# Kernel tuning notes

Hardware: AMD Instinct MI355X
Metric: run time of the kernel (lower is better)

## Reference

```python
import jax, jax.numpy as jnp
import numpy as np

B, S, H, C = 512, 16, 501, 7


def _uniform(k, shape, scale):
    return jax.random.uniform(k, shape, minval=-scale, maxval=scale, dtype=jnp.float32)


def setup_inputs() -> dict:
    key = jax.random.key(0)
    ks = jax.random.split(key, 20)
    s = 1.0 / np.sqrt(H)        # torch default init bound for Linear(H, .) and GRUCell
    se = 1.0 / np.sqrt(2 * H)   # Linear(2H, 1)
    z = jax.random.normal(ks[0], (B, H), jnp.float32)
    # strictly-lower-triangular 0/1 adjacency (DAG, ancestors have smaller index)
    dep = jax.random.randint(ks[1], (B, S, S), 0, 2).astype(jnp.float32)
    dep_graph = dep * jnp.tril(jnp.ones((S, S), jnp.float32), k=-1)
    node_encoding = jax.nn.one_hot(jax.random.randint(ks[2], (B, S), 0, C), C, dtype=jnp.float32)
    return {
        "z": z,
        "dep_graph": dep_graph,
        "node_encoding": node_encoding,
        "W_lin1": _uniform(ks[3], (H, H), s), "b_lin1": _uniform(ks[4], (H,), s),
        "W_vert": _uniform(ks[5], (C, H), s), "b_vert": _uniform(ks[6], (C,), s),
        "W_edge": _uniform(ks[7], (1, 2 * H), se), "b_edge": _uniform(ks[8], (1,), se),
        "W_gate": _uniform(ks[9], (H, H), s), "b_gate": _uniform(ks[10], (H,), s),
        "W_map": _uniform(ks[11], (H, H), s), "b_map": _uniform(ks[12], (H,), s),
        "W_ih": _uniform(ks[13], (3 * H, C), s), "b_ih": _uniform(ks[14], (3 * H,), s),
        "W_hh": _uniform(ks[15], (3 * H, H), s), "b_hh": _uniform(ks[16], (3 * H,), s),
    }


def _forward(z, dep_graph, node_encoding, W_lin1, b_lin1, W_vert, b_vert, W_edge, b_edge,
             W_gate, b_gate, W_map, b_map, W_ih, b_ih, W_hh, b_hh):
    Bs, Ss, _ = dep_graph.shape
    Hs = W_lin1.shape[0]

    def gru(x, h):  # torch.nn.GRUCell math
        gi = x @ W_ih.T + b_ih
        gh = h @ W_hh.T + b_hh
        i_r, i_z, i_n = jnp.split(gi, 3, axis=-1)
        h_r, h_z, h_n = jnp.split(gh, 3, axis=-1)
        r = jax.nn.sigmoid(i_r + h_r)
        u = jax.nn.sigmoid(i_z + h_z)
        n = jnp.tanh(i_n + r * h_n)
        return (1.0 - u) * n + u * h

    col = jnp.arange(Ss)

    def outer_step(carry, idx):
        graph_state, nhs = carry  # nhs: (B, S, H) node_hidden_state
        logits = jax.nn.softmax(graph_state @ W_vert.T + b_vert, axis=-1)  # add_vertex
        x_idx = jax.lax.dynamic_index_in_dim(node_encoding, idx, axis=1, keepdims=False)  # (B, C)
        row0 = jax.lax.dynamic_index_in_dim(dep_graph, idx, axis=1, keepdims=False)       # (B, S)

        def inner_step(ic, t):  # v_j = idx-1, ..., 0 (masked when v_j < 0)
            hv, nhs_i, row, edges = ic
            v_j = idx - 1 - t
            active = v_j >= 0
            vj = jnp.maximum(v_j, 0)
            hidden_j = jax.lax.dynamic_index_in_dim(nhs_i, vj, axis=1, keepdims=False)  # (B, H)
            p = jax.nn.sigmoid(jnp.concatenate([hv, hidden_j], axis=-1) @ W_edge.T + b_edge)  # (B,1)
            is_edge = (p[:, 0] >= 0.5).astype(z.dtype)  # hard threshold, as in source
            # emulates the in-place `ancestors[:, :v_j] = 0` on the dep_graph row
            row_new = jnp.where(col[None, :] < vj, 0.0, row)
            anc = (nhs_i * row_new[:, :, None]).reshape(-1, Hs)  # (B*S, H)
            h_in = (jax.nn.sigmoid(anc @ W_gate.T + b_gate) * (anc @ W_map.T + b_map)
                    ).reshape(Bs, Ss, Hs).sum(axis=1)  # gated-sum message aggregation
            hv_new = gru(x_idx, h_in)
            nhs_new = jax.lax.dynamic_update_index_in_dim(nhs_i, hv_new, idx, axis=1)
            edges = jnp.where(active, edges.at[:, vj].set(is_edge), edges)
            hv = jnp.where(active, hv_new, hv)
            nhs_i = jnp.where(active, nhs_new, nhs_i)
            row = jnp.where(active, row_new, row)
            return (hv, nhs_i, row, edges), None

        edges0 = jnp.zeros((Bs, Ss), z.dtype)
        (hv, nhs2, _, edges), _ = jax.lax.scan(
            inner_step, (graph_state, nhs, row0, edges0), jnp.arange(Ss - 1))
        # index == 0: no ancestors; hv = GRU(x_0, graph_state) (source leaves hv undefined here)
        hv = jnp.where(idx == 0, gru(x_idx, graph_state), hv)
        nhs3 = jax.lax.dynamic_update_index_in_dim(nhs2, hv, idx, axis=1)
        return (hv, nhs3), (logits, edges)

    graph_state0 = z @ W_lin1.T + b_lin1
    nhs0 = jnp.zeros((Bs, Ss, Hs), z.dtype)
    _, (enc, rows) = jax.lax.scan(outer_step, (graph_state0, nhs0), jnp.arange(Ss))
    gen_dep_graph = jnp.transpose(rows, (1, 0, 2))      # (B, S, S)
    gen_node_encoding = jnp.transpose(enc, (1, 0, 2))   # (B, S, C)
    return gen_dep_graph, gen_node_encoding


def reference(z, dep_graph, node_encoding, W_lin1, b_lin1, W_vert, b_vert, W_edge, b_edge,
              W_gate, b_gate, W_map, b_map, W_ih, b_ih, W_hh, b_hh):
    return _forward(z, dep_graph, node_encoding, W_lin1, b_lin1, W_vert, b_vert, W_edge,
                    b_edge, W_gate, b_gate, W_map, b_map, W_ih, b_ih, W_hh, b_hh)
```

## Files before the change

kernel.cpp:

```cpp
#include <hip/hip_runtime.h>
#include <math.h>

#define BB 512
#define SS 16
#define HH 501
#define CC 7
#define OFF_ENC (BB*SS*SS)

#define NBLK 256
#define NTHR 128
#define NTOT (NBLK*NTHR)
#define NBAR 34

#define O_ALIST 0
#define O_ELIST 8192
#define O_CLS   16384
#define O_SYNC  24576
#define O_WLIN  40960
#define O_WPOST (O_WLIN + 262144)
#define O_WHH   (O_WPOST + 524288)
#define O_WDOT  (O_WHH + 786432)
#define O_ROT   (O_WDOT + 8192)
#define SLOT_STRIDE 524288
#define SLOT_Z  0
#define SLOT_IN(t) (1 + (t))
#define SLOT_H(t)  (18 + (t))

typedef __attribute__((ext_vector_type(8))) short bfrag;
typedef __attribute__((ext_vector_type(4))) float ffrag;

__device__ __forceinline__ float sigm(float x) { return 1.f / (1.f + expf(-x)); }

__device__ __forceinline__ unsigned short f2bf(float x) {
    unsigned u = __float_as_uint(x);
    u = u + 0x7fffu + ((u >> 16) & 1u);
    return (unsigned short)(u >> 16);
}
__device__ __forceinline__ float bf2f(unsigned short h) {
    return __uint_as_float(((unsigned)h) << 16);
}

__device__ __forceinline__ void gridbar(int* __restrict__ bars, int id) {
    __syncthreads();
    int* f = bars + id * NBLK;
    if (threadIdx.x == 0)
        __hip_atomic_store(&f[blockIdx.x], 1, __ATOMIC_RELEASE, __HIP_MEMORY_SCOPE_AGENT);
    if (threadIdx.x < 64) {
        for (int i = threadIdx.x; i < NBLK; i += 64)
            while (__hip_atomic_load(&f[i], __ATOMIC_RELAXED, __HIP_MEMORY_SCOPE_AGENT) == 0)
                __builtin_amdgcn_s_sleep(2);
    }
    __syncthreads();
    asm volatile("" ::: "memory");
}

__global__ void k_init(int* bars, int n) {
    int i = blockIdx.x * 256 + threadIdx.x;
    if (i < n) bars[i] = 0;
}

__device__ __forceinline__ void wprep_item(
    int id,
    const float* __restrict__ Wlin1, const float* __restrict__ Wgate,
    const float* __restrict__ Wmap,  const float* __restrict__ Whh,
    const float* __restrict__ Wedge, const float* __restrict__ Wvert,
    unsigned short* __restrict__ wlin, unsigned short* __restrict__ wpost,
    unsigned short* __restrict__ whhf, unsigned short* __restrict__ wdot)
{
    const int slot = id >> 10, rem = id & 1023, s = rem >> 6, lane = rem & 63;
    const int rloc = lane & 15;
    const int k0 = s * 32 + ((lane >> 4) << 3);
    const float* src; unsigned short* dst; int dslot; bool valid;
    if (slot < 32) {
        int row = slot * 16 + rloc; valid = row < HH;
        src = Wlin1 + (size_t)(valid ? row : 0) * HH; dst = wlin; dslot = slot;
    } else if (slot < 96) {
        int p = slot - 32, g = p >> 5, mt = p & 31;
        int row = mt * 16 + rloc; valid = row < HH;
        src = (g ? Wmap : Wgate) + (size_t)(valid ? row : 0) * HH; dst = wpost; dslot = p;
    } else if (slot < 192) {
        int p = slot - 96, g = p >> 5, mt = p & 31;
        int row = mt * 16 + rloc; valid = row < HH;
        src = Whh + (size_t)(g * HH + (valid ? row : 0)) * HH; dst = whhf; dslot = p;
    } else {
        int row = rloc; dst = wdot; dslot = 0;
        if (row < 2)      { src = Wedge + (size_t)row * HH; valid = true; }
        else if (row < 9) { src = Wvert + (size_t)(row - 2) * HH; valid = true; }
        else              { src = Wedge; valid = false; }
    }
    unsigned h[8], l[8];
#pragma unroll
    for (int j = 0; j < 8; ++j) {
        int k = k0 + j;
        float w = (valid && k < HH) ? src[k] : 0.f;
        unsigned short hb = f2bf(w);
        h[j] = hb; l[j] = f2bf(w - bf2f(hb));
    }
    size_t base = ((size_t)dslot * 32 + s * 2) * 512 + lane * 8;
    uint4 uh, ul;
    uh.x = h[0] | (h[1] << 16); uh.y = h[2] | (h[3] << 16);
    uh.z = h[4] | (h[5] << 16); uh.w = h[6] | (h[7] << 16);
    ul.x = l[0] | (l[1] << 16); ul.y = l[2] | (l[3] << 16);
    ul.z = l[4] | (l[5] << 16); ul.w = l[6] | (l[7] << 16);
    *(uint4*)&dst[base] = uh;
    *(uint4*)&dst[base + 512] = ul;
}

__device__ __forceinline__ void prepz_item(
    int id, const float* __restrict__ z,
    unsigned short* __restrict__ zTh, unsigned short* __restrict__ zTl)
{
    const int bb = id >> 6, kc = id & 63, k0 = kc * 8;
    unsigned h[8], l[8];
#pragma unroll
    for (int j = 0; j < 8; ++j) {
        int k = k0 + j;
        float w = (k < HH) ? z[(size_t)bb * HH + k] : 0.f;
        unsigned short hb = f2bf(w);
        h[j] = hb; l[j] = f2bf(w - bf2f(hb));
    }
    uint4 uh, ul;
    uh.x = h[0] | (h[1] << 16); uh.y = h[2] | (h[3] << 16);
    uh.z = h[4] | (h[5] << 16); uh.w = h[6] | (h[7] << 16);
    ul.x = l[0] | (l[1] << 16); ul.y = l[2] | (l[3] << 16);
    ul.z = l[4] | (l[5] << 16); ul.w = l[6] | (l[7] << 16);
    *(uint4*)&zTh[(size_t)bb * 512 + k0] = uh;
    *(uint4*)&zTl[(size_t)bb * 512 + k0] = ul;
}

__device__ __forceinline__ void stage_slot(
    const unsigned short* __restrict__ slot, int cg, uint4* __restrict__ sbu4, int tid)
{
    const uint4* ghi = (const uint4*)(slot + (size_t)cg * 64 * 512);
    const uint4* glo = (const uint4*)(slot + 262144 + (size_t)cg * 64 * 512);
#pragma unroll
    for (int base = 0; base < 4096; base += 1024) {
        uint4 a[8], b[8];
        const int i0 = base + tid;
#pragma unroll
        for (int j = 0; j < 8; ++j) { a[j] = ghi[i0 + j * 128]; b[j] = glo[i0 + j * 128]; }
#pragma unroll
        for (int j = 0; j < 8; ++j) {
            int i = i0 + j * 128, col = i >> 6;
            int d = (col << 6) | ((i & 63) ^ (col & 7));
            sbu4[d] = a[j]; sbu4[4096 + d] = b[j];
        }
    }
}

template<int G>
__device__ __forceinline__ void gemm_core_lds(
    const unsigned short* __restrict__ wf, const uint4* __restrict__ sbu4,
    int mt, int wv, int lane, ffrag* acc)
{
    const char* wp = (const char*)wf + (size_t)lane * 16;
    const int l4 = lane >> 4;
    int colL[2], xm[2];
#pragma unroll
    for (int n = 0; n < 2; ++n) { colL[n] = wv * 32 + n * 16 + (lane & 15); xm[n] = colL[n] & 7; }
#pragma unroll
    for (int s = 0; s < 16; ++s) {
        bfrag bh[2], bl[2];
#pragma unroll
        for (int n = 0; n < 2; ++n) {
            int idx = (colL[n] << 6) | ((s * 4 + l4) ^ xm[n]);
            bh[n] = *(const bfrag*)&sbu4[idx];
            bl[n] = *(const bfrag*)&sbu4[4096 + idx];
        }
#pragma unroll
        for (int g = 0; g < G; ++g) {
            const char* ap = wp + (size_t)((g * 32 + mt) * 32 + s * 2) * 1024;
            bfrag ah = *(const bfrag*)ap;
            bfrag al = *(const bfrag*)(ap + 1024);
#pragma unroll
            for (int n = 0; n < 2; ++n) {
                ffrag* A = acc + g * 2 + n;
                *A = __builtin_amdgcn_mfma_f32_16x16x32_bf16(ah, bh[n], *A, 0, 0, 0);
                *A = __builtin_amdgcn_mfma_f32_16x16x32_bf16(ah, bl[n], *A, 0, 0, 0);
                *A = __builtin_amdgcn_mfma_f32_16x16x32_bf16(al, bh[n], *A, 0, 0, 0);
            }
        }
    }
}

__device__ __forceinline__ void store_T(unsigned short* __restrict__ slot,
                                        int c, int rbase, const float* v) {
    unsigned h[4], l[4];
#pragma unroll
    for (int i = 0; i < 4; ++i) {
        unsigned short hb = f2bf(v[i]);
        h[i] = hb; l[i] = f2bf(v[i] - bf2f(hb));
    }
    uint2 uh, ul;
    uh.x = h[0] | (h[1] << 16); uh.y = h[2] | (h[3] << 16);
    ul.x = l[0] | (l[1] << 16); ul.y = l[2] | (l[3] << 16);
    *(uint2*)&slot[(size_t)c * 512 + rbase] = uh;
    *(uint2*)&slot[262144 + (size_t)c * 512 + rbase] = ul;
}

__device__ __forceinline__ void g0_body(
    int mt, int cg, int lane, int wv, const uint4* __restrict__ sbu4,
    const unsigned short* __restrict__ wlin, const float* __restrict__ blin1,
    float (*hin)[4], unsigned short* __restrict__ dstSlot)
{
    const ffrag fz = {0.f, 0.f, 0.f, 0.f};
    ffrag acc[2]; acc[0] = fz; acc[1] = fz;
    gemm_core_lds<1>(wlin, sbu4, mt, wv, lane, acc);
    const int rbase = mt * 16 + ((lane >> 4) << 2);
#pragma unroll
    for (int n = 0; n < 2; ++n) {
        const int c = cg * 64 + wv * 32 + n * 16 + (lane & 15);
        float v[4];
#pragma unroll
        for (int r = 0; r < 4; ++r) {
            int rr = rbase + r;
            v[r] = (rr < HH) ? acc[n][r] + blin1[rr] : 0.f;
            hin[n][r] = v[r];
        }
        store_T(dstSlot, c, rbase, v);
    }
}

__device__ __forceinline__ void gru_body(
    int mt, int cg, int lane, int wv, const uint4* __restrict__ sbu4,
    const unsigned short* __restrict__ whhf, const float (*hin)[4],
    const int* __restrict__ cls, const float* __restrict__ Wih,
    const float* __restrict__ bih, const float* __restrict__ bhh,
    int idx, unsigned short* __restrict__ dstSlot)
{
    const ffrag fz = {0.f, 0.f, 0.f, 0.f};
    ffrag acc[6];
#pragma unroll
    for (int i = 0; i < 6; ++i) acc[i] = fz;
    gemm_core_lds<3>(whhf, sbu4, mt, wv, lane, acc);
    const int rbase = mt * 16 + ((lane >> 4) << 2);
#pragma unroll
    for (int n = 0; n < 2; ++n) {
        const int c = cg * 64 + wv * 32 + n * 16 + (lane & 15);
        const int cc = cls[idx * BB + c];
        float v[4];
#pragma unroll
        for (int r = 0; r < 4; ++r) {
            int rr = rbase + r;
            if (rr < HH) {
                float ar  = acc[0 * 2 + n][r];
                float az  = acc[1 * 2 + n][r];
                float an2 = acc[2 * 2 + n][r];
                float rgt = sigm(Wih[(size_t)rr * CC + cc] + bih[rr] + ar + bhh[rr]);
                float ugt = sigm(Wih[(size_t)(HH + rr) * CC + cc] + bih[HH + rr] + az + bhh[HH + rr]);
                float ngt = tanhf(Wih[(size_t)(2 * HH + rr) * CC + cc] + bih[2 * HH + rr]
                                  + rgt * (an2 + bhh[2 * HH + rr]));
                v[r] = (1.f - ugt) * ngt + ugt * hin[n][r];
            } else v[r] = 0.f;
        }
        store_T(dstSlot, c, rbase, v);
    }
}

__device__ __forceinline__ void post_body(
    int mt, int cg, int lane, int wv, const uint4* __restrict__ sbu4,
    const unsigned short* __restrict__ wpostf,
    const float* __restrict__ bgate, const float* __restrict__ bmap,
    const float* __restrict__ dep, int idx,
    float (*hin)[4], unsigned short* __restrict__ dstSlot)
{
    const ffrag fz = {0.f, 0.f, 0.f, 0.f};
    ffrag acc[4];
#pragma unroll
    for (int i = 0; i < 4; ++i) acc[i] = fz;
    gemm_core_lds<2>(wpostf, sbu4, mt, wv, lane, acc);
    const int rbase = mt * 16 + ((lane >> 4) << 2);
#pragma unroll
    for (int n = 0; n < 2; ++n) {
        const int c = cg * 64 + wv * 32 + n * 16 + (lane & 15);
        const float d = dep[(size_t)c * (SS * SS) + (idx + 1) * SS + idx];
        float v[4];
#pragma unroll
        for (int r = 0; r < 4; ++r) {
            int rr = rbase + r;
            if (rr < HH) {
                float bg = bgate[rr], bm = bmap[rr];
                float cv = sigm(bg) * bm;
                float f = sigm(acc[0 * 2 + n][r] + bg) * (acc[1 * 2 + n][r] + bm);
                v[r] = (d != 0.f) ? (f + 15.f * cv) : (16.f * cv);
            } else v[r] = 0.f;
            hin[n][r] = v[r];
        }
        store_T(dstSlot, c, rbase, v);
    }
}

__device__ __forceinline__ void dots_body(
    int blk8, int tid, int lane, int wv, const uint4* __restrict__ sbu4,
    const unsigned short* __restrict__ wdot, const float* __restrict__ bvert,
    const float* __restrict__ bedge, float* __restrict__ Alist, float* __restrict__ Elist,
    int idx, float* __restrict__ out, float (*dls)[65])
{
    const ffrag fz = {0.f, 0.f, 0.f, 0.f};
    ffrag acc[2]; acc[0] = fz; acc[1] = fz;
    const char* wp = (const char*)wdot + (size_t)lane * 16;
    const int l4 = lane >> 4;
    int colL[2], xm[2];
#pragma unroll
    for (int n = 0; n < 2; ++n) { colL[n] = wv * 32 + n * 16 + (lane & 15); xm[n] = colL[n] & 7; }
#pragma unroll
    for (int s = 0; s < 16; ++s) {
        bfrag ah = *(const bfrag*)(wp + (size_t)(s * 2) * 1024);
        bfrag al = *(const bfrag*)(wp + (size_t)(s * 2 + 1) * 1024);
#pragma unroll
        for (int n = 0; n < 2; ++n) {
            int idx4 = (colL[n] << 6) | ((s * 4 + l4) ^ xm[n]);
            bfrag bh = *(const bfrag*)&sbu4[idx4];
            bfrag bl = *(const bfrag*)&sbu4[4096 + idx4];
            acc[n] = __builtin_amdgcn_mfma_f32_16x16x32_bf16(ah, bh, acc[n], 0, 0, 0);
            acc[n] = __builtin_amdgcn_mfma_f32_16x16x32_bf16(ah, bl, acc[n], 0, 0, 0);
            acc[n] = __builtin_amdgcn_mfma_f32_16x16x32_bf16(al, bh, acc[n], 0, 0, 0);
        }
    }
#pragma unroll
    for (int n = 0; n < 2; ++n)
#pragma unroll
        for (int r = 0; r < 4; ++r)
            dls[((lane >> 4) << 2) + r][wv * 32 + n * 16 + (lane & 15)] = acc[n][r];
    __syncthreads();
    if (tid < 64) {
        const int b = blk8 * 64 + tid;
        float v[9];
#pragma unroll
        for (int j = 0; j < 9; ++j) v[j] = dls[j][tid];
        if (idx >= 0) { Alist[idx * BB + b] = v[0]; Elist[idx * BB + b] = v[1]; }
        if (idx <= SS - 2) {
            float lv[CC], mx = -1e30f;
#pragma unroll
            for (int c = 0; c < CC; ++c) { lv[c] = v[2 + c] + bvert[c]; mx = fmaxf(mx, lv[c]); }
            float sum = 0.f, ev[CC];
#pragma unroll
            for (int c = 0; c < CC; ++c) { ev[c] = expf(lv[c] - mx); sum += ev[c]; }
            float inv = 1.f / sum;
#pragma unroll
            for (int c = 0; c < CC; ++c)
                out[OFF_ENC + ((size_t)b * SS + (idx + 1)) * CC + c] = ev[c] * inv;
        }
        if (idx >= 1) {
            float be = bedge[0];
            float aprev = Alist[(idx - 1) * BB + b], eprev = Elist[(idx - 1) * BB + b];
            out[(size_t)b * SS * SS + idx * SS + (idx - 1)] =
                (aprev + eprev + be >= 0.f) ? 1.f : 0.f;
            for (int vj = 0; vj <= idx - 2; ++vj)
                out[(size_t)b * SS * SS + idx * SS + vj] =
                    (v[0] + Elist[vj * BB + b] + be >= 0.f) ? 1.f : 0.f;
        }
    }
    __syncthreads();
}

__global__ __launch_bounds__(NTHR, 1) void k_fused(
    const float* z, const float* dep, const float* xenc,
    const float* Wlin1, const float* blin1,
    const float* Wvert, const float* bvert,
    const float* Wedge, const float* bedge,
    const float* Wgate, const float* bgate,
    const float* Wmap,  const float* bmap,
    const float* Wih,   const float* bih,
    const float* Whh,   const float* bhh,
    float* out, float* ws)
{
    __shared__ uint4 sbu4[8192];
    __shared__ float dls[16][65];

    float* Alist = ws + O_ALIST;
    float* Elist = ws + O_ELIST;
    int*   cls   = (int*)(ws + O_CLS);
    int*   bars  = (int*)(ws + O_SYNC);
    unsigned short* wlin  = (unsigned short*)(ws + O_WLIN);
    unsigned short* wpost = (unsigned short*)(ws + O_WPOST);
    unsigned short* whhf  = (unsigned short*)(ws + O_WHH);
    unsigned short* wdot  = (unsigned short*)(ws + O_WDOT);
    unsigned short* rot   = (unsigned short*)(ws + O_ROT);

    const int bid = blockIdx.x, tid = threadIdx.x;
    const int lane = tid & 63, wv = tid >> 6;
    const int mt = bid >> 3, cg = bid & 7;
    const int gt = bid * NTHR + tid;
    float hinreg[2][4];
    int barid = 0;

    for (int i = gt; i < 193 * 1024; i += NTOT)
        wprep_item(i, Wlin1, Wgate, Wmap, Whh, Wedge, Wvert, wlin, wpost, whhf, wdot);
    {
        unsigned short* zslot = rot + (size_t)SLOT_Z * SLOT_STRIDE;
        for (int i = gt; i < 32768; i += NTOT)
            prepz_item(i, z, zslot, zslot + 262144);
    }
    for (int i = gt; i < 8192; i += NTOT) {
        int sI = i >> 9, bb = i & 511;
        const float* xp = xenc + ((size_t)bb * SS + sI) * CC;
        int cv = 0;
#pragma unroll
        for (int cc = 0; cc < CC; ++cc) if (xp[cc] > 0.5f) cv = cc;
        cls[sI * BB + bb] = cv;
    }
    if (bid < 8) {
        float4 z4 = make_float4(0.f, 0.f, 0.f, 0.f);
        float4* o4 = (float4*)out + (size_t)bid * 4096;
        for (int i = tid; i < 4096; i += NTHR) o4[i] = z4;
    }
    gridbar(bars, barid++);

    stage_slot(rot + (size_t)SLOT_Z * SLOT_STRIDE, cg, sbu4, tid);
    __syncthreads();
    g0_body(mt, cg, lane, wv, sbu4, wlin, blin1, hinreg,
            rot + (size_t)SLOT_IN(0) * SLOT_STRIDE);
    gridbar(bars, barid++);

    for (int idx = 0; idx < SS; ++idx) {
        stage_slot(rot + (size_t)SLOT_IN(idx) * SLOT_STRIDE, cg, sbu4, tid);
        __syncthreads();
        gru_body(mt, cg, lane, wv, sbu4, whhf, hinreg, cls, Wih, bih, bhh,
                 idx, rot + (size_t)SLOT_H(idx) * SLOT_STRIDE);
        if (bid < 8 && idx == 0)
            dots_body(cg, tid, lane, wv, sbu4, wdot, bvert, bedge,
                      Alist, Elist, -1, out, dls);
        gridbar(bars, barid++);
        stage_slot(rot + (size_t)SLOT_H(idx) * SLOT_STRIDE, cg, sbu4, tid);
        __syncthreads();
        if (idx < SS - 1)
            post_body(mt, cg, lane, wv, sbu4, wpost, bgate, bmap, dep, idx,
                      hinreg, rot + (size_t)SLOT_IN(idx + 1) * SLOT_STRIDE);
        if (bid < 8)
            dots_body(cg, tid, lane, wv, sbu4, wdot, bvert, bedge,
                      Alist, Elist, idx, out, dls);
        if (idx < SS - 1) gridbar(bars, barid++);
    }
}

extern "C" void kernel_launch(void* const* d_in, const int* in_sizes, int n_in,
                              void* d_out, int out_size, void* d_ws, size_t ws_size,
                              hipStream_t stream)
{
    const float* z     = (const float*)d_in[0];
    const float* dep   = (const float*)d_in[1];
    const float* xenc  = (const float*)d_in[2];
    const float* Wlin1 = (const float*)d_in[3];
    const float* blin1 = (const float*)d_in[4];
    const float* Wvert = (const float*)d_in[5];
    const float* bvert = (const float*)d_in[6];
    const float* Wedge = (const float*)d_in[7];
    const float* bedge = (const float*)d_in[8];
    const float* Wgate = (const float*)d_in[9];
    const float* bgate = (const float*)d_in[10];
    const float* Wmap  = (const float*)d_in[11];
    const float* bmap  = (const float*)d_in[12];
    const float* Wih   = (const float*)d_in[13];
    const float* bih   = (const float*)d_in[14];
    const float* Whh   = (const float*)d_in[15];
    const float* bhh   = (const float*)d_in[16];
    float* out = (float*)d_out;
    float* ws  = (float*)d_ws;

    int* bars = (int*)(ws + O_SYNC);
    k_init<<<NBAR, 256, 0, stream>>>(bars, NBAR * NBLK);
    k_fused<<<NBLK, NTHR, 0, stream>>>(z, dep, xenc, Wlin1, blin1, Wvert, bvert,
                                       Wedge, bedge, Wgate, bgate, Wmap, bmap,
                                       Wih, bih, Whh, bhh, out, ws);
}
```

Before: 1.339 ms.

## Split persistent kernel into 512 GEMM blocks plus 8 dot blocks reading B from global

Removes the 128KB LDS staging of the activation slot. Each GEMM block now reads its B fragments straight from global/L2 and handles 32 columns instead of 64, so the grid grows to 512 GEMM blocks plus 8 dedicated blocks for the vertex/edge dot products. Launch bounds allow 2 blocks per CU, and the sync area offset and barrier init size grow to match. This trades the LDS fill and per-block serialization for more parallel blocks and concurrent dot work. It risks more global read traffic and costlier grid barriers with 520 participants.

```diff
diff --git a/kernel.cpp b/kernel.cpp
--- a/kernel.cpp
+++ b/kernel.cpp
@@ -7,7 +7,7 @@
 #define CC 7
 #define OFF_ENC (BB*SS*SS)
 
-#define NBLK 256
+#define NBLK 520
 #define NTHR 128
 #define NTOT (NBLK*NTHR)
 #define NBAR 34
@@ -16,7 +16,7 @@
 #define O_ELIST 8192
 #define O_CLS   16384
 #define O_SYNC  24576
-#define O_WLIN  40960
+#define O_WLIN  49152
 #define O_WPOST (O_WLIN + 262144)
 #define O_WHH   (O_WPOST + 524288)
 #define O_WDOT  (O_WHH + 786432)
@@ -107,8 +107,7 @@
 }
 
 __device__ __forceinline__ void prepz_item(
-    int id, const float* __restrict__ z,
-    unsigned short* __restrict__ zTh, unsigned short* __restrict__ zTl)
+    int id, const float* __restrict__ z, unsigned short* __restrict__ zslot)
 {
     const int bb = id >> 6, kc = id & 63, k0 = kc * 8;
     unsigned h[8], l[8];
@@ -124,61 +123,29 @@
     uh.z = h[4] | (h[5] << 16); uh.w = h[6] | (h[7] << 16);
     ul.x = l[0] | (l[1] << 16); ul.y = l[2] | (l[3] << 16);
     ul.z = l[4] | (l[5] << 16); ul.w = l[6] | (l[7] << 16);
-    *(uint4*)&zTh[(size_t)bb * 512 + k0] = uh;
-    *(uint4*)&zTl[(size_t)bb * 512 + k0] = ul;
-}
-
-__device__ __forceinline__ void stage_slot(
-    const unsigned short* __restrict__ slot, int cg, uint4* __restrict__ sbu4, int tid)
-{
-    const uint4* ghi = (const uint4*)(slot + (size_t)cg * 64 * 512);
-    const uint4* glo = (const uint4*)(slot + 262144 + (size_t)cg * 64 * 512);
-#pragma unroll
-    for (int base = 0; base < 4096; base += 1024) {
-        uint4 a[8], b[8];
-        const int i0 = base + tid;
-#pragma unroll
-        for (int j = 0; j < 8; ++j) { a[j] = ghi[i0 + j * 128]; b[j] = glo[i0 + j * 128]; }
-#pragma unroll
-        for (int j = 0; j < 8; ++j) {
-            int i = i0 + j * 128, col = i >> 6;
-            int d = (col << 6) | ((i & 63) ^ (col & 7));
-            sbu4[d] = a[j]; sbu4[4096 + d] = b[j];
-        }
-    }
+    *(uint4*)&zslot[(size_t)bb * 512 + k0] = uh;
+    *(uint4*)&zslot[262144 + (size_t)bb * 512 + k0] = ul;
 }
 
 template<int G>
-__device__ __forceinline__ void gemm_core_lds(
-    const unsigned short* __restrict__ wf, const uint4* __restrict__ sbu4,
-    int mt, int wv, int lane, ffrag* acc)
+__device__ __forceinline__ void gemm_core_g(
+    const unsigned short* __restrict__ wf, const unsigned short* __restrict__ bslot,
+    int mt, int col, int lane, ffrag* acc)
 {
     const char* wp = (const char*)wf + (size_t)lane * 16;
-    const int l4 = lane >> 4;
-    int colL[2], xm[2];
-#pragma unroll
-    for (int n = 0; n < 2; ++n) { colL[n] = wv * 32 + n * 16 + (lane & 15); xm[n] = colL[n] & 7; }
+    const unsigned short* bp = bslot + (size_t)col * 512 + ((lane >> 4) << 3);
 #pragma unroll
     for (int s = 0; s < 16; ++s) {
-        bfrag bh[2], bl[2];
-#pragma unroll
-        for (int n = 0; n < 2; ++n) {
-            int idx = (colL[n] << 6) | ((s * 4 + l4) ^ xm[n]);
-            bh[n] = *(const bfrag*)&sbu4[idx];
-            bl[n] = *(const bfrag*)&sbu4[4096 + idx];
-        }
+        bfrag bh = *(const bfrag*)(bp + s * 32);
+        bfrag bl = *(const bfrag*)(bp + 262144 + s * 32);
 #pragma unroll
         for (int g = 0; g < G; ++g) {
             const char* ap = wp + (size_t)((g * 32 + mt) * 32 + s * 2) * 1024;
             bfrag ah = *(const bfrag*)ap;
             bfrag al = *(const bfrag*)(ap + 1024);
-#pragma unroll
-            for (int n = 0; n < 2; ++n) {
-                ffrag* A = acc + g * 2 + n;
-                *A = __builtin_amdgcn_mfma_f32_16x16x32_bf16(ah, bh[n], *A, 0, 0, 0);
-                *A = __builtin_amdgcn_mfma_f32_16x16x32_bf16(ah, bl[n], *A, 0, 0, 0);
-                *A = __builtin_amdgcn_mfma_f32_16x16x32_bf16(al, bh[n], *A, 0, 0, 0);
-            }
+            acc[g] = __builtin_amdgcn_mfma_f32_16x16x32_bf16(ah, bh, acc[g], 0, 0, 0);
+            acc[g] = __builtin_amdgcn_mfma_f32_16x16x32_bf16(ah, bl, acc[g], 0, 0, 0);
+            acc[g] = __builtin_amdgcn_mfma_f32_16x16x32_bf16(al, bh, acc[g], 0, 0, 0);
         }
     }
 }
@@ -199,99 +166,89 @@
 }
 
 __device__ __forceinline__ void g0_body(
-    int mt, int cg, int lane, int wv, const uint4* __restrict__ sbu4,
+    int mt, int col, int lane,
+    const unsigned short* __restrict__ bslot,
     const unsigned short* __restrict__ wlin, const float* __restrict__ blin1,
-    float (*hin)[4], unsigned short* __restrict__ dstSlot)
+    float* hin, unsigned short* __restrict__ dstSlot)
 {
     const ffrag fz = {0.f, 0.f, 0.f, 0.f};
-    ffrag acc[2]; acc[0] = fz; acc[1] = fz;
-    gemm_core_lds<1>(wlin, sbu4, mt, wv, lane, acc);
+    ffrag acc[1]; acc[0] = fz;
+    gemm_core_g<1>(wlin, bslot, mt, col, lane, acc);
     const int rbase = mt * 16 + ((lane >> 4) << 2);
-#pragma unroll
-    for (int n = 0; n < 2; ++n) {
-        const int c = cg * 64 + wv * 32 + n * 16 + (lane & 15);
-        float v[4];
-#pragma unroll
-        for (int r = 0; r < 4; ++r) {
-            int rr = rbase + r;
-            v[r] = (rr < HH) ? acc[n][r] + blin1[rr] : 0.f;
-            hin[n][r] = v[r];
-        }
-        store_T(dstSlot, c, rbase, v);
-    }
+    float v[4];
+#pragma unroll
+    for (int r = 0; r < 4; ++r) {
+        int rr = rbase + r;
+        v[r] = (rr < HH) ? acc[0][r] + blin1[rr] : 0.f;
+        hin[r] = v[r];
+    }
+    store_T(dstSlot, col, rbase, v);
 }
 
 __device__ __forceinline__ void gru_body(
-    int mt, int cg, int lane, int wv, const uint4* __restrict__ sbu4,
-    const unsigned short* __restrict__ whhf, const float (*hin)[4],
+    int mt, int col, int lane,
+    const unsigned short* __restrict__ bslot,
+    const unsigned short* __restrict__ whhf, const float* hin,
     const int* __restrict__ cls, const float* __restrict__ Wih,
     const float* __restrict__ bih, const float* __restrict__ bhh,
     int idx, unsigned short* __restrict__ dstSlot)
 {
     const ffrag fz = {0.f, 0.f, 0.f, 0.f};
-    ffrag acc[6];
-#pragma unroll
-    for (int i = 0; i < 6; ++i) acc[i] = fz;
-    gemm_core_lds<3>(whhf, sbu4, mt, wv, lane, acc);
+    ffrag acc[3];
+#pragma unroll
+    for (int i = 0; i < 3; ++i) acc[i] = fz;
+    gemm_core_g<3>(whhf, bslot, mt, col, lane, acc);
     const int rbase = mt * 16 + ((lane >> 4) << 2);
-#pragma unroll
-    for (int n = 0; n < 2; ++n) {
-        const int c = cg * 64 + wv * 32 + n * 16 + (lane & 15);
-        const int cc = cls[idx * BB + c];
-        float v[4];
-#pragma unroll
-        for (int r = 0; r < 4; ++r) {
-            int rr = rbase + r;
-            if (rr < HH) {
-                float ar  = acc[0 * 2 + n][r];
-                float az  = acc[1 * 2 + n][r];
-                float an2 = acc[2 * 2 + n][r];
-                float rgt = sigm(Wih[(size_t)rr * CC + cc] + bih[rr] + ar + bhh[rr]);
-                float ugt = sigm(Wih[(size_t)(HH + rr) * CC + cc] + bih[HH + rr] + az + bhh[HH + rr]);
-                float ngt = tanhf(Wih[(size_t)(2 * HH + rr) * CC + cc] + bih[2 * HH + rr]
-                                  + rgt * (an2 + bhh[2 * HH + rr]));
-                v[r] = (1.f - ugt) * ngt + ugt * hin[n][r];
-            } else v[r] = 0.f;
-        }
-        store_T(dstSlot, c, rbase, v);
-    }
+    const int cc = cls[idx * BB + col];
+    float v[4];
+#pragma unroll
+    for (int r = 0; r < 4; ++r) {
+        int rr = rbase + r;
+        if (rr < HH) {
+            float ar  = acc[0][r];
+            float az  = acc[1][r];
+            float an2 = acc[2][r];
+            float rgt = sigm(Wih[(size_t)rr * CC + cc] + bih[rr] + ar + bhh[rr]);
+            float ugt = sigm(Wih[(size_t)(HH + rr) * CC + cc] + bih[HH + rr] + az + bhh[HH + rr]);
+            float ngt = tanhf(Wih[(size_t)(2 * HH + rr) * CC + cc] + bih[2 * HH + rr]
+                              + rgt * (an2 + bhh[2 * HH + rr]));
+            v[r] = (1.f - ugt) * ngt + ugt * hin[r];
+        } else v[r] = 0.f;
+    }
+    store_T(dstSlot, col, rbase, v);
 }
 
 __device__ __forceinline__ void post_body(
-    int mt, int cg, int lane, int wv, const uint4* __restrict__ sbu4,
+    int mt, int col, int lane,
+    const unsigned short* __restrict__ bslot,
     const unsigned short* __restrict__ wpostf,
     const float* __restrict__ bgate, const float* __restrict__ bmap,
     const float* __restrict__ dep, int idx,
-    float (*hin)[4], unsigned short* __restrict__ dstSlot)
+    float* hin, unsigned short* __restrict__ dstSlot)
 {
     const ffrag fz = {0.f, 0.f, 0.f, 0.f};
-    ffrag acc[4];
-#pragma unroll
-    for (int i = 0; i < 4; ++i) acc[i] = fz;
-    gemm_core_lds<2>(wpostf, sbu4, mt, wv, lane, acc);
+    ffrag acc[2]; acc[0] = fz; acc[1] = fz;
+    gemm_core_g<2>(wpostf, bslot, mt, col, lane, acc);
     const int rbase = mt * 16 + ((lane >> 4) << 2);
-#pragma unroll
-    for (int n = 0; n < 2; ++n) {
-        const int c = cg * 64 + wv * 32 + n * 16 + (lane & 15);
-        const float d = dep[(size_t)c * (SS * SS) + (idx + 1) * SS + idx];
-        float v[4];
-#pragma unroll
-        for (int r = 0; r < 4; ++r) {
-            int rr = rbase + r;
-            if (rr < HH) {
-                float bg = bgate[rr], bm = bmap[rr];
-                float cv = sigm(bg) * bm;
-                float f = sigm(acc[0 * 2 + n][r] + bg) * (acc[1 * 2 + n][r] + bm);
-                v[r] = (d != 0.f) ? (f + 15.f * cv) : (16.f * cv);
-            } else v[r] = 0.f;
-            hin[n][r] = v[r];
-        }
-        store_T(dstSlot, c, rbase, v);
-    }
+    const float d = dep[(size_t)col * (SS * SS) + (idx + 1) * SS + idx];
+    float v[4];
+#pragma unroll
+    for (int r = 0; r < 4; ++r) {
+        int rr = rbase + r;
+        if (rr < HH) {
+            float bg = bgate[rr], bm = bmap[rr];
+            float cv = sigm(bg) * bm;
+            float f = sigm(acc[0][r] + bg) * (acc[1][r] + bm);
+            v[r] = (d != 0.f) ? (f + 15.f * cv) : (16.f * cv);
+        } else v[r] = 0.f;
+        hin[r] = v[r];
+    }
+    store_T(dstSlot, col, rbase, v);
 }
 
 __device__ __forceinline__ void dots_body(
-    int blk8, int tid, int lane, int wv, const uint4* __restrict__ sbu4,
+    int blk8, int tid, int lane, int wv,
+    const unsigned short* __restrict__ bslot,
     const unsigned short* __restrict__ wdot, const float* __restrict__ bvert,
     const float* __restrict__ bedge, float* __restrict__ Alist, float* __restrict__ Elist,
     int idx, float* __restrict__ out, float (*dls)[65])
@@ -300,18 +257,18 @@
     ffrag acc[2]; acc[0] = fz; acc[1] = fz;
     const char* wp = (const char*)wdot + (size_t)lane * 16;
     const int l4 = lane >> 4;
-    int colL[2], xm[2];
-#pragma unroll
-    for (int n = 0; n < 2; ++n) { colL[n] = wv * 32 + n * 16 + (lane & 15); xm[n] = colL[n] & 7; }
+    int colL[2];
+#pragma unroll
+    for (int n = 0; n < 2; ++n) colL[n] = blk8 * 64 + wv * 32 + n * 16 + (lane & 15);
 #pragma unroll
     for (int s = 0; s < 16; ++s) {
         bfrag ah = *(const bfrag*)(wp + (size_t)(s * 2) * 1024);
         bfrag al = *(const bfrag*)(wp + (size_t)(s * 2 + 1) * 1024);
 #pragma unroll
         for (int n = 0; n < 2; ++n) {
-            int idx4 = (colL[n] << 6) | ((s * 4 + l4) ^ xm[n]);
-            bfrag bh = *(const bfrag*)&sbu4[idx4];
-            bfrag bl = *(const bfrag*)&sbu4[4096 + idx4];
+            const unsigned short* bp = bslot + (size_t)colL[n] * 512 + (l4 << 3) + s * 32;
+            bfrag bh = *(const bfrag*)bp;
+            bfrag bl = *(const bfrag*)(bp + 262144);
             acc[n] = __builtin_amdgcn_mfma_f32_16x16x32_bf16(ah, bh, acc[n], 0, 0, 0);
             acc[n] = __builtin_amdgcn_mfma_f32_16x16x32_bf16(ah, bl, acc[n], 0, 0, 0);
             acc[n] = __builtin_amdgcn_mfma_f32_16x16x32_bf16(al, bh, acc[n], 0, 0, 0);
@@ -321,7 +278,7 @@
     for (int n = 0; n < 2; ++n)
 #pragma unroll
         for (int r = 0; r < 4; ++r)
-            dls[((lane >> 4) << 2) + r][wv * 32 + n * 16 + (lane & 15)] = acc[n][r];
+            dls[(l4 << 2) + r][wv * 32 + n * 16 + (lane & 15)] = acc[n][r];
     __syncthreads();
     if (tid < 64) {
         const int b = blk8 * 64 + tid;
@@ -354,7 +311,7 @@
     __syncthreads();
 }
 
-__global__ __launch_bounds__(NTHR, 1) void k_fused(
+__global__ __launch_bounds__(NTHR, 2) void k_fused(
     const float* z, const float* dep, const float* xenc,
     const float* Wlin1, const float* blin1,
     const float* Wvert, const float* bvert,
@@ -365,7 +322,6 @@
     const float* Whh,   const float* bhh,
     float* out, float* ws)
 {
-    __shared__ uint4 sbu4[8192];
     __shared__ float dls[16][65];
 
     float* Alist = ws + O_ALIST;
@@ -380,9 +336,12 @@
 
     const int bid = blockIdx.x, tid = threadIdx.x;
     const int lane = tid & 63, wv = tid >> 6;
-    const int mt = bid >> 3, cg = bid & 7;
+    const bool gemm = bid < 512;
+    const int mt = bid & 31, c32 = bid >> 5;
+    const int col = c32 * 32 + wv * 16 + (lane & 15);
+    const int blk8 = bid - 512;
     const int gt = bid * NTHR + tid;
-    float hinreg[2][4];
+    float hinreg[4];
     int barid = 0;
 
     for (int i = gt; i < 193 * 1024; i += NTOT)
@@ -390,7 +349,7 @@
     {
         unsigned short* zslot = rot + (size_t)SLOT_Z * SLOT_STRIDE;
         for (int i = gt; i < 32768; i += NTOT)
-            prepz_item(i, z, zslot, zslot + 262144);
+            prepz_item(i, z, zslot);
     }
     for (int i = gt; i < 8192; i += NTOT) {
         int sI = i >> 9, bb = i & 511;
@@ -400,36 +359,36 @@
         for (int cc = 0; cc < CC; ++cc) if (xp[cc] > 0.5f) cv = cc;
         cls[sI * BB + bb] = cv;
     }
-    if (bid < 8) {
+    {
         float4 z4 = make_float4(0.f, 0.f, 0.f, 0.f);
-        float4* o4 = (float4*)out + (size_t)bid * 4096;
-        for (int i = tid; i < 4096; i += NTHR) o4[i] = z4;
+        float4* o4 = (float4*)out;
+        for (int i = gt; i < 32768; i += NTOT) o4[i] = z4;
     }
     gridbar(bars, barid++);
 
-    stage_slot(rot + (size_t)SLOT_Z * SLOT_STRIDE, cg, sbu4, tid);
-    __syncthreads();
-    g0_body(mt, cg, lane, wv, sbu4, wlin, blin1, hinreg,
-            rot + (size_t)SLOT_IN(0) * SLOT_STRIDE);
+    if (gemm)
+        g0_body(mt, col, lane, rot + (size_t)SLOT_Z * SLOT_STRIDE, wlin, blin1,
+                hinreg, rot + (size_t)SLOT_IN(0) * SLOT_STRIDE);
     gridbar(bars, barid++);
 
     for (int idx = 0; idx < SS; ++idx) {
-        stage_slot(rot + (size_t)SLOT_IN(idx) * SLOT_STRIDE, cg, sbu4, tid);
-        __syncthreads();
-        gru_body(mt, cg, lane, wv, sbu4, whhf, hinreg, cls, Wih, bih, bhh,
-                 idx, rot + (size_t)SLOT_H(idx) * SLOT_STRIDE);
-        if (bid < 8 && idx == 0)
-            dots_body(cg, tid, lane, wv, sbu4, wdot, bvert, bedge,
-                      Alist, Elist, -1, out, dls);
+        if (gemm)
+            gru_body(mt, col, lane, rot + (size_t)SLOT_IN(idx) * SLOT_STRIDE,
+                     whhf, hinreg, cls, Wih, bih, bhh,
+                     idx, rot + (size_t)SLOT_H(idx) * SLOT_STRIDE);
+        else if (idx == 0)
+            dots_body(blk8, tid, lane, wv, rot + (size_t)SLOT_IN(0) * SLOT_STRIDE,
+                      wdot, bvert, bedge, Alist, Elist, -1, out, dls);
         gridbar(bars, barid++);
-        stage_slot(rot + (size_t)SLOT_H(idx) * SLOT_STRIDE, cg, sbu4, tid);
-        __syncthreads();
-        if (idx < SS - 1)
-            post_body(mt, cg, lane, wv, sbu4, wpost, bgate, bmap, dep, idx,
-                      hinreg, rot + (size_t)SLOT_IN(idx + 1) * SLOT_STRIDE);
-        if (bid < 8)
-            dots_body(cg, tid, lane, wv, sbu4, wdot, bvert, bedge,
-                      Alist, Elist, idx, out, dls);
+        if (gemm) {
+            if (idx < SS - 1)
+                post_body(mt, col, lane, rot + (size_t)SLOT_H(idx) * SLOT_STRIDE,
+                          wpost, bgate, bmap, dep, idx,
+                          hinreg, rot + (size_t)SLOT_IN(idx + 1) * SLOT_STRIDE);
+        } else {
+            dots_body(blk8, tid, lane, wv, rot + (size_t)SLOT_H(idx) * SLOT_STRIDE,
+                      wdot, bvert, bedge, Alist, Elist, idx, out, dls);
+        }
         if (idx < SS - 1) gridbar(bars, barid++);
     }
 }
@@ -459,7 +418,7 @@
     float* ws  = (float*)d_ws;
 
     int* bars = (int*)(ws + O_SYNC);
-    k_init<<<NBAR, 256, 0, stream>>>(bars, NBAR * NBLK);
+    k_init<<<(NBAR * NBLK + 255) / 256, 256, 0, stream>>>(bars, NBAR * NBLK);
     k_fused<<<NBLK, NTHR, 0, stream>>>(z, dep, xenc, Wlin1, blin1, Wvert, bvert,
                                        Wedge, bedge, Wgate, bgate, Wmap, bmap,
                                        Wih, bih, Whh, bhh, out, ws);
```

Result: slower. 1.444 ms (+7.9%).
